# Performance work log

Hardware: AMD Instinct MI355X
Metric: run time of the kernel (lower is better)

Reference implementation:

```python
import jax, jax.numpy as jnp
import numpy as np

D_MODEL = 1024
N_HEADS = 16
MAX_SEQ_LEN = 2048

def setup_inputs() -> dict:
    key = jax.random.key(0)
    ks = jax.random.split(key, 4)
    B, L, D = 2, 2048, D_MODEL
    s = 0.02
    x = jax.random.normal(ks[0], (B, L, D), dtype=jnp.float32)
    qkv_w = jax.random.normal(ks[1], (D, 3 * D), dtype=jnp.float32) * s
    qkv_b = jnp.zeros((3 * D,), dtype=jnp.float32)
    proj_w = jax.random.normal(ks[2], (D, D), dtype=jnp.float32) * s
    proj_b = jnp.zeros((D,), dtype=jnp.float32)
    bias_table = jax.random.normal(ks[3], (2 * MAX_SEQ_LEN - 1, N_HEADS), dtype=jnp.float32) * s
    return {"x": x, "qkv_w": qkv_w, "qkv_b": qkv_b, "proj_w": proj_w, "proj_b": proj_b, "bias_table": bias_table}

def reference(x, qkv_w, qkv_b, proj_w, proj_b, bias_table):
    B, L, D = x.shape
    H = N_HEADS
    dk = D // H
    scale = dk ** -0.5
    # fused qkv projection: (B,L,3,H,dk)
    qkv = (x @ qkv_w + qkv_b).reshape(B, L, 3, H, dk)
    q = qkv[:, :, 0].transpose(0, 2, 1, 3)  # (B,H,L,dk)
    k = qkv[:, :, 1].transpose(0, 2, 1, 3)
    v = qkv[:, :, 2].transpose(0, 2, 1, 3)
    attn = jnp.einsum("bhqd,bhkd->bhqk", q, k) * scale  # (B,H,L,L)
    # relative position bias gather (Swin-style)
    coords = jnp.arange(L)
    rel_idx = coords[None, :] - coords[:, None] + (MAX_SEQ_LEN - 1)  # (L,L)
    rel_bias = bias_table[rel_idx]  # (L,L,H)
    attn = attn + rel_bias.transpose(2, 0, 1)[None]  # (B,H,L,L)
    attn = jax.nn.softmax(attn, axis=-1)
    out = jnp.einsum("bhqk,bhkd->bhqd", attn, v)  # (B,H,L,dk)
    out = out.transpose(0, 2, 1, 3).reshape(B, L, D)
    return out @ proj_w + proj_b
```

## Files before the change

### kernel.cpp

```cpp
#include <hip/hip_runtime.h>
#include <stdint.h>

typedef __attribute__((ext_vector_type(4))) float    f32x4;
typedef f32x4 __attribute__((aligned(4)))   f32x4u;
typedef __attribute__((ext_vector_type(8))) short    bf16x8;
typedef __attribute__((ext_vector_type(2))) uint32_t u32x2;
typedef __attribute__((ext_vector_type(4))) uint32_t u32x4;

#define MFMA16(a,b,c) __builtin_amdgcn_mfma_f32_16x16x32_bf16((a),(b),(c),0,0,0)

__device__ __forceinline__ uint16_t f2bf(float f){
  uint32_t u = __float_as_uint(f);
  return (uint16_t)((u + 0x7FFFu + ((u >> 16) & 1u)) >> 16);
}

__device__ __forceinline__ uint32_t pk_bf16(float lo, float hi){
  uint32_t r; asm("v_cvt_pk_bf16_f32 %0, %1, %2" : "=v"(r) : "v"(lo), "v"(hi)); return r;
}

__device__ __forceinline__ float fast_exp2(float x){
  float r; asm("v_exp_f32 %0, %1" : "=v"(r) : "v"(x)); return r;
}
__device__ __forceinline__ float fast_log2(float x){
  float r; asm("v_log_f32 %0, %1" : "=v"(r) : "v"(x)); return r;
}

__device__ __forceinline__ float bfl(uint32_t u){ return __uint_as_float(u << 16); }
__device__ __forceinline__ float bfh(uint32_t u){ return __uint_as_float(u & 0xffff0000u); }

__device__ __forceinline__ void gload16(const uint16_t* g, uint16_t* l){
  __builtin_amdgcn_global_load_lds((const __attribute__((address_space(1))) uint32_t*)g,
                                   (__attribute__((address_space(3))) uint32_t*)l, 16, 0, 0);
}

__global__ void k_cvtb(const float* __restrict__ in, uint16_t* __restrict__ out,
                       const float* __restrict__ btab, float* __restrict__ bias_t){
  const int bx = blockIdx.x;
  if (bx < 4096){
    const size_t i = (size_t)(bx*256 + threadIdx.x) * 4;
    const f32x4 v = *(const f32x4*)(in + i);
    u32x2 pk = {pk_bf16(v[0], v[1]), pk_bf16(v[2], v[3])};
    *(u32x2*)(out + i) = pk;
  } else {
    const int i = (bx - 4096)*256 + threadIdx.x;
    if (i < 4095*16) bias_t[(i & 15)*4096 + (i >> 4)] = btab[i] * 1.4426950408889634f;
  }
}

__global__ void k_tcvt(const float* __restrict__ in, uint16_t* __restrict__ out, int K, int N){
  __shared__ float tile[64][65];
  const int k0 = blockIdx.y*64, n0 = blockIdx.x*64;
  const int tc = threadIdx.x & 63, tr = threadIdx.x >> 6;
  #pragma unroll
  for (int p=0;p<16;p++){ int r = p*4 + tr; tile[r][tc] = in[(size_t)(k0+r)*N + n0 + tc]; }
  __syncthreads();
  #pragma unroll
  for (int p=0;p<16;p++){ int r = p*4 + tr; out[(size_t)(n0+r)*K + k0 + tc] = f2bf(tile[tc][r]); }
}

__global__ __launch_bounds__(256, 2) void k_gemm(
    const uint16_t* __restrict__ A, const uint16_t* __restrict__ Bt,
    const float* __restrict__ bias,
    uint16_t* __restrict__ qo, uint16_t* __restrict__ ko, uint16_t* __restrict__ vto)
{
  __shared__ __align__(16) uint16_t at[128*64];
  __shared__ __align__(16) uint16_t bt[128*64];
  const int tid = threadIdx.x;
  const int lane = tid & 63, w = tid >> 6;
  const int g = lane >> 4, li = lane & 15;
  const int wr = w >> 1, wc = w & 1;
  const int m0 = blockIdx.y * 128, n0 = blockIdx.x * 128;

  f32x4 acc[4][4] = {};

  const int srow = tid >> 3;
  const int scg  = (tid & 7) ^ (srow & 7);

  for (int kt_ = 0; kt_ < 16; kt_++){
    const int kk = kt_*64;
    __syncthreads();
    #pragma unroll
    for (int j = 0; j < 4; j++){
      gload16(A  + (size_t)(m0 + j*32 + srow)*1024 + kk + scg*8, at + (j*256+tid)*8);
      gload16(Bt + (size_t)(n0 + j*32 + srow)*1024 + kk + scg*8, bt + (j*256+tid)*8);
    }
    asm volatile("s_waitcnt vmcnt(0)" ::: "memory");
    __syncthreads();

    bf16x8 af[2][4], bfr[2][4];
    #pragma unroll
    for (int mi=0; mi<4; mi++){
      int row = wr*64 + mi*16 + li, sw = row & 7;
      af[0][mi] = *(const bf16x8*)(at + row*64 + ((g     ^ sw)*8));
      af[1][mi] = *(const bf16x8*)(at + row*64 + (((4+g) ^ sw)*8));
    }
    #pragma unroll
    for (int ni=0; ni<4; ni++){
      int row = wc*64 + ni*16 + li, sw = row & 7;
      bfr[0][ni] = *(const bf16x8*)(bt + row*64 + ((g     ^ sw)*8));
      bfr[1][ni] = *(const bf16x8*)(bt + row*64 + (((4+g) ^ sw)*8));
    }
    #pragma unroll
    for (int s=0; s<2; s++)
      #pragma unroll
      for (int mi=0; mi<4; mi++)
        #pragma unroll
        for (int ni=0; ni<4; ni++)
          acc[mi][ni] = MFMA16(af[s][mi], bfr[s][ni], acc[mi][ni]);
  }

  #pragma unroll
  for (int ni=0; ni<4; ni++){
    const int c = n0 + wc*64 + ni*16 + li;
    const float bv = bias[c];
    const int which = c >> 10, cc = c & 1023;
    const int h = cc >> 6, d = cc & 63;
    #pragma unroll
    for (int mi=0; mi<4; mi++){
      const int trow = m0 + wr*64 + mi*16 + g*4;
      const int b_ = trow >> 11, lcl = trow & 2047;
      const f32x4 v4 = acc[mi][ni];
      if (which == 0){
        uint16_t* dst = qo + (((size_t)(b_*16 + h)*2048 + lcl)*64 + d);
        #pragma unroll
        for (int r=0;r<4;r++) dst[(size_t)r*64] = f2bf((v4[r] + bv) * 0.18033688011112042f);
      } else if (which == 1){
        uint16_t* dst = ko + (((size_t)(b_*16 + h)*2048 + lcl)*64 + d);
        #pragma unroll
        for (int r=0;r<4;r++) dst[(size_t)r*64] = f2bf(v4[r] + bv);
      } else {
        u32x2 pk = {pk_bf16(v4[0]+bv, v4[1]+bv), pk_bf16(v4[2]+bv, v4[3]+bv)};
        *(u32x2*)(vto + (((size_t)(b_*16 + h)*64 + d)*2048 + lcl)) = pk;
      }
    }
  }
}

__global__ __launch_bounds__(256, 2) void k_gemm2(
    const uint16_t* __restrict__ A, const uint16_t* __restrict__ Bt,
    const float* __restrict__ bias, float* __restrict__ outf)
{
  __shared__ __align__(16) uint16_t at[128*64];
  __shared__ __align__(16) uint16_t bt[64*64];
  const int tid = threadIdx.x;
  const int lane = tid & 63, w = tid >> 6;
  const int g = lane >> 4, li = lane & 15;
  const int wr = w >> 1, wc = w & 1;
  const int m0 = blockIdx.y * 128, n0 = blockIdx.x * 64;

  f32x4 acc[4][2] = {};
  const int srow = tid >> 3;
  const int scg  = (tid & 7) ^ (srow & 7);

  for (int kt_ = 0; kt_ < 16; kt_++){
    const int kk = kt_*64;
    __syncthreads();
    #pragma unroll
    for (int j = 0; j < 4; j++)
      gload16(A  + (size_t)(m0 + j*32 + srow)*1024 + kk + scg*8, at + (j*256+tid)*8);
    #pragma unroll
    for (int j = 0; j < 2; j++)
      gload16(Bt + (size_t)(n0 + j*32 + srow)*1024 + kk + scg*8, bt + (j*256+tid)*8);
    asm volatile("s_waitcnt vmcnt(0)" ::: "memory");
    __syncthreads();

    bf16x8 af[2][4], bfr[2][2];
    #pragma unroll
    for (int mi=0; mi<4; mi++){
      int row = wr*64 + mi*16 + li, sw = row & 7;
      af[0][mi] = *(const bf16x8*)(at + row*64 + ((g     ^ sw)*8));
      af[1][mi] = *(const bf16x8*)(at + row*64 + (((4+g) ^ sw)*8));
    }
    #pragma unroll
    for (int ni=0; ni<2; ni++){
      int row = wc*32 + ni*16 + li, sw = row & 7;
      bfr[0][ni] = *(const bf16x8*)(bt + row*64 + ((g     ^ sw)*8));
      bfr[1][ni] = *(const bf16x8*)(bt + row*64 + (((4+g) ^ sw)*8));
    }
    #pragma unroll
    for (int s=0; s<2; s++)
      #pragma unroll
      for (int mi=0; mi<4; mi++)
        #pragma unroll
        for (int ni=0; ni<2; ni++)
          acc[mi][ni] = MFMA16(af[s][mi], bfr[s][ni], acc[mi][ni]);
  }

  #pragma unroll
  for (int ni=0; ni<2; ni++){
    const int c = n0 + wc*32 + ni*16 + li;
    const float bv = bias[c];
    #pragma unroll
    for (int mi=0; mi<4; mi++){
      const int trow = m0 + wr*64 + mi*16 + g*4;
      float* dst = outf + (size_t)trow*1024 + c;
      const f32x4 v4 = acc[mi][ni];
      #pragma unroll
      for (int r=0;r<4;r++) dst[(size_t)r*1024] = v4[r] + bv;
    }
  }
}

__device__ __forceinline__ void attn_tile(
    int t, bool last, int tid, int g, int li, int srow, int scg,
    const uint16_t* kbase, const uint16_t* vbase, const float* bb,
    const uint16_t* ktc, uint16_t* ktn, const uint16_t* vtc, uint16_t* vtn, uint16_t* pl,
    const bf16x8 (&qf)[2][2], bf16x8 ones,
    f32x4 (&o)[4][2], f32x4 (&o4)[2], float& mrun0, float& mrun1)
{
  const int kv0 = t*64;

  f32x4 bv5[5];
  #pragma unroll
  for (int j=0;j<5;j++)
    bv5[j] = *(const f32x4u*)(bb + kv0 + (j-1)*16 + g*4 - li);
  asm volatile("" ::: "memory");

  if (!last){
    const int kv1 = kv0 + 64;
    gload16(kbase + (size_t)(kv1+srow)*64 + scg*8,         ktn + tid*8);
    gload16(kbase + (size_t)(kv1+srow+32)*64 + scg*8,      ktn + 2048 + tid*8);
    gload16(vbase + (size_t)srow*2048 + kv1 + scg*8,       vtn + tid*8);
    gload16(vbase + (size_t)(srow+32)*2048 + kv1 + scg*8,  vtn + 2048 + tid*8);
    asm volatile("s_waitcnt vmcnt(9)" ::: "memory");
  } else {
    asm volatile("s_waitcnt vmcnt(5)" ::: "memory");
  }
  __builtin_amdgcn_s_barrier();

  f32x4 sa[4][2];
  __builtin_amdgcn_s_setprio(1);
  #pragma unroll
  for (int mf=0; mf<4; mf++){
    const int row = mf*16 + li, sw = row & 7;
    bf16x8 a0 = *(const bf16x8*)(ktc + row*64 + ((g     ^ sw)*8));
    bf16x8 a1 = *(const bf16x8*)(ktc + row*64 + (((4+g) ^ sw)*8));
    #pragma unroll
    for (int c=0;c<2;c++){
      f32x4 cfr = {};
      cfr = MFMA16(a0, qf[c][0], cfr);
      cfr = MFMA16(a1, qf[c][1], cfr);
      sa[mf][c] = cfr;
    }
  }
  __builtin_amdgcn_s_setprio(0);

  float t0 = -__builtin_inff(), t1 = -__builtin_inff();
  #pragma unroll
  for (int mf=0; mf<4; mf++){
    sa[mf][0] += bv5[mf+1];
    sa[mf][1] += bv5[mf];
    #pragma unroll
    for (int r=0; r<4; r++){
      t0 = fmaxf(t0, sa[mf][0][r]);
      t1 = fmaxf(t1, sa[mf][1][r]);
    }
  }

  const int ok = (t0 <= mrun0 + 8.f) && (t1 <= mrun1 + 8.f);
  if (!__all(ok)){
    float r0 = t0, r1 = t1;
    r0 = fmaxf(r0, __shfl_xor(r0, 16)); r0 = fmaxf(r0, __shfl_xor(r0, 32));
    r1 = fmaxf(r1, __shfl_xor(r1, 16)); r1 = fmaxf(r1, __shfl_xor(r1, 32));
    const float mn0 = fmaxf(mrun0, r0), mn1 = fmaxf(mrun1, r1);
    const float a0 = fast_exp2(mrun0 - mn0), a1 = fast_exp2(mrun1 - mn1);
    #pragma unroll
    for (int mf=0; mf<4; mf++){ o[mf][0] *= a0; o[mf][1] *= a1; }
    o4[0] *= a0; o4[1] *= a1;
    mrun0 = mn0; mrun1 = mn1;
  }

  bf16x8 av[2][4];
  #pragma unroll
  for (int s=0; s<2; s++)
    #pragma unroll
    for (int mf=0; mf<4; mf++){
      const int row = mf*16 + li, sw = row & 7;
      av[s][mf] = *(const bf16x8*)(vtc + row*64 + (((4*s+g) ^ sw)*8));
    }

  const int swp2 = 2*(li & 7);
  #pragma unroll
  for (int c=0;c<2;c++){
    const float mr = c ? mrun1 : mrun0;
    #pragma unroll
    for (int mf=0; mf<4; mf++){
      float p0 = fast_exp2(sa[mf][c][0] - mr);
      float p1 = fast_exp2(sa[mf][c][1] - mr);
      float p2 = fast_exp2(sa[mf][c][2] - mr);
      float p3 = fast_exp2(sa[mf][c][3] - mr);
      u32x2 pk = {pk_bf16(p0,p1), pk_bf16(p2,p3)};
      *(u32x2*)(pl + li*64 + (((4*mf+g) ^ swp2)*4)) = pk;
    }
    __builtin_amdgcn_s_setprio(1);
    #pragma unroll
    for (int s=0; s<2; s++){
      bf16x8 pb = *(const bf16x8*)(pl + li*64 + (((8*s+2*g) ^ swp2)*4));
      o4[c] = MFMA16(ones, pb, o4[c]);
      #pragma unroll
      for (int mf=0; mf<4; mf++)
        o[mf][c] = MFMA16(av[s][mf], pb, o[mf][c]);
    }
    __builtin_amdgcn_s_setprio(0);
  }
  __builtin_amdgcn_s_barrier();
}

__global__ __launch_bounds__(256, 2) void k_attn(
    const uint16_t* __restrict__ qg, const uint16_t* __restrict__ kg,
    const uint16_t* __restrict__ vg, const float* __restrict__ biast,
    uint16_t* __restrict__ opart, float* __restrict__ spart)
{
  __shared__ __align__(16) uint16_t kt[2][64*64];
  __shared__ __align__(16) uint16_t vt[2][64*64];
  __shared__ __align__(16) uint16_t pt[4][16*64];
  const int tid = threadIdx.x;
  const int lane = tid & 63, w = tid >> 6;
  const int g = lane >> 4, li = lane & 15;
  const int bh = blockIdx.y, h = bh & 15, b_ = bh >> 4;
  const int id = blockIdx.x;
  const int split = id & 1, qxi = id >> 1;
  const int qw = qxi*128 + w*32;
  const int tg0 = split*16;

  bf16x8 qf[2][2];
  #pragma unroll
  for (int c=0;c<2;c++){
    const uint16_t* qp = qg + ((size_t)bh*2048 + qw + c*16 + li)*64 + g*8;
    qf[c][0] = *(const bf16x8*)(qp);
    qf[c][1] = *(const bf16x8*)(qp + 32);
  }
  bf16x8 ones = (bf16x8)(short)0;
  if (li == 0){ const short v = (short)0x3F80; ones = (bf16x8){v,v,v,v,v,v,v,v}; }

  f32x4 o[4][2] = {};
  f32x4 o4[2] = {};
  float mrun0 = -__builtin_inff(), mrun1 = -__builtin_inff();

  const uint16_t* kbase = kg + (size_t)bh*(2048*64);
  const uint16_t* vbase = vg + (size_t)bh*(64*2048);
  const int srow = tid >> 3;
  const int scg  = (tid & 7) ^ (srow & 7);
  const float* bb = biast + h*4096 + 2047 - qw;
  uint16_t* pl = &pt[w][0];

  const int kvp = tg0*64;
  gload16(kbase + (size_t)(kvp+srow)*64 + scg*8,        &kt[0][tid*8]);
  gload16(kbase + (size_t)(kvp+srow+32)*64 + scg*8,     &kt[0][2048 + tid*8]);
  gload16(vbase + (size_t)srow*2048 + kvp + scg*8,      &vt[0][tid*8]);
  gload16(vbase + (size_t)(srow+32)*2048 + kvp + scg*8, &vt[0][2048 + tid*8]);

  for (int tt = 0; tt < 16; tt += 2){
    attn_tile(tg0+tt,   false,      tid, g, li, srow, scg, kbase, vbase, bb,
              &kt[0][0], &kt[1][0], &vt[0][0], &vt[1][0], pl,
              qf, ones, o, o4, mrun0, mrun1);
    attn_tile(tg0+tt+1, tt == 14,   tid, g, li, srow, scg, kbase, vbase, bb,
              &kt[1][0], &kt[0][0], &vt[1][0], &vt[0][0], pl,
              qf, ones, o, o4, mrun0, mrun1);
  }

  const float ls0 = __shfl(o4[0][0], li);
  const float ls1 = __shfl(o4[1][0], li);
  const float inv0 = 1.0f / ls0, inv1 = 1.0f / ls1;
  const float sv0 = mrun0 + fast_log2(ls0);
  const float sv1 = mrun1 + fast_log2(ls1);
  #pragma unroll
  for (int c=0;c<2;c++){
    const float inv = c ? inv1 : inv0;
    const int token = b_*2048 + qw + c*16 + li;
    if (g == 0) spart[split*65536 + token*16 + h] = c ? sv1 : sv0;
    uint16_t* dst = opart + ((size_t)(split*4096 + token))*1024 + h*64;
    #pragma unroll
    for (int mf=0; mf<4; mf++){
      u32x2 pk = {pk_bf16(o[mf][c][0]*inv, o[mf][c][1]*inv),
                  pk_bf16(o[mf][c][2]*inv, o[mf][c][3]*inv)};
      *(u32x2*)(dst + mf*16 + g*4) = pk;
    }
  }
}

__global__ void k_merge(const uint16_t* __restrict__ op, const float* __restrict__ sp,
                        uint16_t* __restrict__ ao){
  const int gid = blockIdx.x*256 + threadIdx.x;
  const int token = gid >> 7, col0 = (gid & 127) * 8, h = col0 >> 6;
  const float s0 = sp[token*16 + h], s1 = sp[65536 + token*16 + h];
  const float sm = fmaxf(s0, s1);
  float w0 = fast_exp2(s0 - sm), w1 = fast_exp2(s1 - sm);
  const float inv = 1.0f / (w0 + w1);
  w0 *= inv; w1 *= inv;
  const size_t i0 = (size_t)token*1024 + col0;
  const u32x4 a = *(const u32x4*)(op + i0);
  const u32x4 b = *(const u32x4*)(op + (size_t)4096*1024 + i0);
  u32x4 r;
  #pragma unroll
  for (int j=0;j<4;j++){
    const float e0 = w0*bfl(a[j]) + w1*bfl(b[j]);
    const float e1 = w0*bfh(a[j]) + w1*bfh(b[j]);
    r[j] = pk_bf16(e0, e1);
  }
  *(u32x4*)(ao + i0) = r;
}

extern "C" void kernel_launch(void* const* d_in, const int* in_sizes, int n_in,
                              void* d_out, int out_size, void* d_ws, size_t ws_size,
                              hipStream_t stream)
{
  const float* x      = (const float*)d_in[0];
  const float* qkv_w  = (const float*)d_in[1];
  const float* qkv_b  = (const float*)d_in[2];
  const float* proj_w = (const float*)d_in[3];
  const float* proj_b = (const float*)d_in[4];
  const float* btab   = (const float*)d_in[5];
  float* out = (float*)d_out;

  char* p = (char*)d_ws;
  uint16_t* x_bf    = (uint16_t*)(p);
  uint16_t* qkv_wt  = (uint16_t*)(p + 8388608);
  uint16_t* proj_wt = (uint16_t*)(p + 14680064);
  uint16_t* q_buf   = (uint16_t*)(p + 16777216);
  uint16_t* k_buf   = (uint16_t*)(p + 25165824);
  uint16_t* vt_buf  = (uint16_t*)(p + 33554432);
  uint16_t* ao_buf  = (uint16_t*)(p + 41943040);
  float*    bias_t  = (float*)   (p + 50331648);

  uint16_t* o_part = (uint16_t*)d_out;
  float*    s_part = (float*)p;

  k_cvtb <<<dim3(4352),  dim3(256), 0, stream>>>(x, x_bf, btab, bias_t);
  k_tcvt <<<dim3(48,16), dim3(256), 0, stream>>>(qkv_w,  qkv_wt,  1024, 3072);
  k_tcvt <<<dim3(16,16), dim3(256), 0, stream>>>(proj_w, proj_wt, 1024, 1024);

  k_gemm   <<<dim3(24,32), dim3(256), 0, stream>>>(x_bf, qkv_wt, qkv_b, q_buf, k_buf, vt_buf);
  k_attn   <<<dim3(32,32), dim3(256), 0, stream>>>(q_buf, k_buf, vt_buf, bias_t, o_part, s_part);
  k_merge  <<<dim3(2048),  dim3(256), 0, stream>>>(o_part, s_part, ao_buf);
  k_gemm2  <<<dim3(16,32), dim3(256), 0, stream>>>(ao_buf, proj_wt, proj_b, out);
}
```

Measured before the change: 124.4 us.

## Fuse split-KV merge into output projection GEMM A-tile load

Removes the separate merge kernel. The projection GEMM now reads both partial attention outputs and their log-sum-exp values directly, combines them in registers and writes the merged bf16 tile into shared memory. This drops one launch and the write and re-read of the merged activation buffer. In exchange, each of the 16 column blocks recomputes the merge for its rows, and the A-tile load becomes a synchronous register path instead of an async global-to-LDS load. Workspace buffers are also relocated so the partials no longer live in the output buffer.

```diff
diff --git a/kernel.cpp b/kernel.cpp
--- a/kernel.cpp
+++ b/kernel.cpp
@@ -137,7 +137,8 @@
 }
 
 __global__ __launch_bounds__(256, 2) void k_gemm2(
-    const uint16_t* __restrict__ A, const uint16_t* __restrict__ Bt,
+    const uint16_t* __restrict__ op, const float* __restrict__ sp,
+    const uint16_t* __restrict__ Bt,
     const float* __restrict__ bias, float* __restrict__ outf)
 {
   __shared__ __align__(16) uint16_t at[128*64];
@@ -156,11 +157,29 @@
     const int kk = kt_*64;
     __syncthreads();
     #pragma unroll
-    for (int j = 0; j < 4; j++)
-      gload16(A  + (size_t)(m0 + j*32 + srow)*1024 + kk + scg*8, at + (j*256+tid)*8);
-    #pragma unroll
     for (int j = 0; j < 2; j++)
       gload16(Bt + (size_t)(n0 + j*32 + srow)*1024 + kk + scg*8, bt + (j*256+tid)*8);
+    #pragma unroll
+    for (int j = 0; j < 4; j++){
+      const int token = m0 + j*32 + srow;
+      const float s0 = sp[token*16 + kt_];
+      const float s1 = sp[65536 + token*16 + kt_];
+      const float sm = fmaxf(s0, s1);
+      float w0 = fast_exp2(s0 - sm), w1 = fast_exp2(s1 - sm);
+      const float winv = 1.0f / (w0 + w1);
+      w0 *= winv; w1 *= winv;
+      const uint16_t* ap = op + (size_t)token*1024 + kk + scg*8;
+      const u32x4 a = *(const u32x4*)(ap);
+      const u32x4 b = *(const u32x4*)(ap + 4194304);
+      u32x4 r;
+      #pragma unroll
+      for (int e=0;e<4;e++){
+        const float e0 = w0*bfl(a[e]) + w1*bfl(b[e]);
+        const float e1 = w0*bfh(a[e]) + w1*bfh(b[e]);
+        r[e] = pk_bf16(e0, e1);
+      }
+      *(u32x4*)(at + (j*256+tid)*8) = r;
+    }
     asm volatile("s_waitcnt vmcnt(0)" ::: "memory");
     __syncthreads();
 
@@ -379,28 +398,6 @@
   }
 }
 
-__global__ void k_merge(const uint16_t* __restrict__ op, const float* __restrict__ sp,
-                        uint16_t* __restrict__ ao){
-  const int gid = blockIdx.x*256 + threadIdx.x;
-  const int token = gid >> 7, col0 = (gid & 127) * 8, h = col0 >> 6;
-  const float s0 = sp[token*16 + h], s1 = sp[65536 + token*16 + h];
-  const float sm = fmaxf(s0, s1);
-  float w0 = fast_exp2(s0 - sm), w1 = fast_exp2(s1 - sm);
-  const float inv = 1.0f / (w0 + w1);
-  w0 *= inv; w1 *= inv;
-  const size_t i0 = (size_t)token*1024 + col0;
-  const u32x4 a = *(const u32x4*)(op + i0);
-  const u32x4 b = *(const u32x4*)(op + (size_t)4096*1024 + i0);
-  u32x4 r;
-  #pragma unroll
-  for (int j=0;j<4;j++){
-    const float e0 = w0*bfl(a[j]) + w1*bfl(b[j]);
-    const float e1 = w0*bfh(a[j]) + w1*bfh(b[j]);
-    r[j] = pk_bf16(e0, e1);
-  }
-  *(u32x4*)(ao + i0) = r;
-}
-
 extern "C" void kernel_launch(void* const* d_in, const int* in_sizes, int n_in,
                               void* d_out, int out_size, void* d_ws, size_t ws_size,
                               hipStream_t stream)
@@ -416,15 +413,13 @@
   char* p = (char*)d_ws;
   uint16_t* x_bf    = (uint16_t*)(p);
   uint16_t* qkv_wt  = (uint16_t*)(p + 8388608);
-  uint16_t* proj_wt = (uint16_t*)(p + 14680064);
   uint16_t* q_buf   = (uint16_t*)(p + 16777216);
   uint16_t* k_buf   = (uint16_t*)(p + 25165824);
   uint16_t* vt_buf  = (uint16_t*)(p + 33554432);
-  uint16_t* ao_buf  = (uint16_t*)(p + 41943040);
+  uint16_t* proj_wt = (uint16_t*)(p + 41943040);
+  float*    s_part  = (float*)   (p + 44040192);
   float*    bias_t  = (float*)   (p + 50331648);
-
-  uint16_t* o_part = (uint16_t*)d_out;
-  float*    s_part = (float*)p;
+  uint16_t* o_part  = (uint16_t*)(p);
 
   k_cvtb <<<dim3(4352),  dim3(256), 0, stream>>>(x, x_bf, btab, bias_t);
   k_tcvt <<<dim3(48,16), dim3(256), 0, stream>>>(qkv_w,  qkv_wt,  1024, 3072);
@@ -432,6 +427,5 @@
 
   k_gemm   <<<dim3(24,32), dim3(256), 0, stream>>>(x_bf, qkv_wt, qkv_b, q_buf, k_buf, vt_buf);
   k_attn   <<<dim3(32,32), dim3(256), 0, stream>>>(q_buf, k_buf, vt_buf, bias_t, o_part, s_part);
-  k_merge  <<<dim3(2048),  dim3(256), 0, stream>>>(o_part, s_part, ao_buf);
-  k_gemm2  <<<dim3(16,32), dim3(256), 0, stream>>>(ao_buf, proj_wt, proj_b, out);
-}
+  k_gemm2  <<<dim3(16,32), dim3(256), 0, stream>>>(o_part, s_part, proj_wt, proj_b, out);
+}
```

Result: slower. 157.0 us (+26.2%).

## Double-buffer LDS tiles in QKV GEMM to overlap global loads with MFMA

Applied to the files above, without the earlier changes.

Splits the A and B shared-memory tiles into two buffers and issues the global-to-LDS loads for the next K tile before computing on the current one. It waits only for the older loads with a partial vmcnt wait, and uses raw s_barrier calls in place of __syncthreads. This hides global load latency behind the MFMA work. In exchange LDS use doubles to 64KB per block, which may limit the 2-blocks-per-CU target, and the barrier and waitcnt ordering has to be right for correctness.

```diff
diff --git a/kernel.cpp b/kernel.cpp
--- a/kernel.cpp
+++ b/kernel.cpp
@@ -63,8 +63,8 @@
     const float* __restrict__ bias,
     uint16_t* __restrict__ qo, uint16_t* __restrict__ ko, uint16_t* __restrict__ vto)
 {
-  __shared__ __align__(16) uint16_t at[128*64];
-  __shared__ __align__(16) uint16_t bt[128*64];
+  __shared__ __align__(16) uint16_t at[2][128*64];
+  __shared__ __align__(16) uint16_t bt[2][128*64];
   const int tid = threadIdx.x;
   const int lane = tid & 63, w = tid >> 6;
   const int g = lane >> 4, li = lane & 15;
@@ -76,29 +76,41 @@
   const int srow = tid >> 3;
   const int scg  = (tid & 7) ^ (srow & 7);
 
+  #pragma unroll
+  for (int j = 0; j < 4; j++){
+    gload16(A  + (size_t)(m0 + j*32 + srow)*1024 + scg*8, &at[0][(j*256+tid)*8]);
+    gload16(Bt + (size_t)(n0 + j*32 + srow)*1024 + scg*8, &bt[0][(j*256+tid)*8]);
+  }
+
   for (int kt_ = 0; kt_ < 16; kt_++){
-    const int kk = kt_*64;
-    __syncthreads();
-    #pragma unroll
-    for (int j = 0; j < 4; j++){
-      gload16(A  + (size_t)(m0 + j*32 + srow)*1024 + kk + scg*8, at + (j*256+tid)*8);
-      gload16(Bt + (size_t)(n0 + j*32 + srow)*1024 + kk + scg*8, bt + (j*256+tid)*8);
-    }
-    asm volatile("s_waitcnt vmcnt(0)" ::: "memory");
-    __syncthreads();
+    const int cur = kt_ & 1;
+    if (kt_ < 15){
+      const int kk1 = (kt_+1)*64;
+      #pragma unroll
+      for (int j = 0; j < 4; j++){
+        gload16(A  + (size_t)(m0 + j*32 + srow)*1024 + kk1 + scg*8, &at[cur^1][(j*256+tid)*8]);
+        gload16(Bt + (size_t)(n0 + j*32 + srow)*1024 + kk1 + scg*8, &bt[cur^1][(j*256+tid)*8]);
+      }
+      asm volatile("s_waitcnt vmcnt(8)" ::: "memory");
+    } else {
+      asm volatile("s_waitcnt vmcnt(0)" ::: "memory");
+    }
+    __builtin_amdgcn_s_barrier();
+    const uint16_t* atc = &at[cur][0];
+    const uint16_t* btc = &bt[cur][0];
 
     bf16x8 af[2][4], bfr[2][4];
     #pragma unroll
     for (int mi=0; mi<4; mi++){
       int row = wr*64 + mi*16 + li, sw = row & 7;
-      af[0][mi] = *(const bf16x8*)(at + row*64 + ((g     ^ sw)*8));
-      af[1][mi] = *(const bf16x8*)(at + row*64 + (((4+g) ^ sw)*8));
+      af[0][mi] = *(const bf16x8*)(atc + row*64 + ((g     ^ sw)*8));
+      af[1][mi] = *(const bf16x8*)(atc + row*64 + (((4+g) ^ sw)*8));
     }
     #pragma unroll
     for (int ni=0; ni<4; ni++){
       int row = wc*64 + ni*16 + li, sw = row & 7;
-      bfr[0][ni] = *(const bf16x8*)(bt + row*64 + ((g     ^ sw)*8));
-      bfr[1][ni] = *(const bf16x8*)(bt + row*64 + (((4+g) ^ sw)*8));
+      bfr[0][ni] = *(const bf16x8*)(btc + row*64 + ((g     ^ sw)*8));
+      bfr[1][ni] = *(const bf16x8*)(btc + row*64 + (((4+g) ^ sw)*8));
     }
     #pragma unroll
     for (int s=0; s<2; s++)
@@ -107,6 +119,7 @@
         #pragma unroll
         for (int ni=0; ni<4; ni++)
           acc[mi][ni] = MFMA16(af[s][mi], bfr[s][ni], acc[mi][ni]);
+    __builtin_amdgcn_s_barrier();
   }
 
   #pragma unroll
```

After: 132.8 us. 1.07x slower.

## Remove split-KV attention and merge kernel, process full key range per block

Applied to the files above, without the earlier changes.

The attention kernel no longer splits the key dimension into two halves with partial outputs and log-sum-exp values. Each block now loops over all 32 key tiles and writes the normalized bf16 output directly, so the separate merge kernel and its partial-buffer traffic go away. The cost is half as many attention blocks (512 instead of 1024 on 256 CUs at 2 blocks per CU), which lowers occupancy and parallelism, and each block runs a longer serial loop.

```diff
diff --git a/kernel.cpp b/kernel.cpp
--- a/kernel.cpp
+++ b/kernel.cpp
@@ -5,7 +5,6 @@
 typedef f32x4 __attribute__((aligned(4)))   f32x4u;
 typedef __attribute__((ext_vector_type(8))) short    bf16x8;
 typedef __attribute__((ext_vector_type(2))) uint32_t u32x2;
-typedef __attribute__((ext_vector_type(4))) uint32_t u32x4;
 
 #define MFMA16(a,b,c) __builtin_amdgcn_mfma_f32_16x16x32_bf16((a),(b),(c),0,0,0)
 
@@ -21,12 +20,6 @@
 __device__ __forceinline__ float fast_exp2(float x){
   float r; asm("v_exp_f32 %0, %1" : "=v"(r) : "v"(x)); return r;
 }
-__device__ __forceinline__ float fast_log2(float x){
-  float r; asm("v_log_f32 %0, %1" : "=v"(r) : "v"(x)); return r;
-}
-
-__device__ __forceinline__ float bfl(uint32_t u){ return __uint_as_float(u << 16); }
-__device__ __forceinline__ float bfh(uint32_t u){ return __uint_as_float(u & 0xffff0000u); }
 
 __device__ __forceinline__ void gload16(const uint16_t* g, uint16_t* l){
   __builtin_amdgcn_global_load_lds((const __attribute__((address_space(1))) uint32_t*)g,
@@ -309,7 +302,7 @@
 __global__ __launch_bounds__(256, 2) void k_attn(
     const uint16_t* __restrict__ qg, const uint16_t* __restrict__ kg,
     const uint16_t* __restrict__ vg, const float* __restrict__ biast,
-    uint16_t* __restrict__ opart, float* __restrict__ spart)
+    uint16_t* __restrict__ outp)
 {
   __shared__ __align__(16) uint16_t kt[2][64*64];
   __shared__ __align__(16) uint16_t vt[2][64*64];
@@ -318,10 +311,7 @@
   const int lane = tid & 63, w = tid >> 6;
   const int g = lane >> 4, li = lane & 15;
   const int bh = blockIdx.y, h = bh & 15, b_ = bh >> 4;
-  const int id = blockIdx.x;
-  const int split = id & 1, qxi = id >> 1;
-  const int qw = qxi*128 + w*32;
-  const int tg0 = split*16;
+  const int qw = blockIdx.x*128 + w*32;
 
   bf16x8 qf[2][2];
   #pragma unroll
@@ -344,17 +334,16 @@
   const float* bb = biast + h*4096 + 2047 - qw;
   uint16_t* pl = &pt[w][0];
 
-  const int kvp = tg0*64;
-  gload16(kbase + (size_t)(kvp+srow)*64 + scg*8,        &kt[0][tid*8]);
-  gload16(kbase + (size_t)(kvp+srow+32)*64 + scg*8,     &kt[0][2048 + tid*8]);
-  gload16(vbase + (size_t)srow*2048 + kvp + scg*8,      &vt[0][tid*8]);
-  gload16(vbase + (size_t)(srow+32)*2048 + kvp + scg*8, &vt[0][2048 + tid*8]);
-
-  for (int tt = 0; tt < 16; tt += 2){
-    attn_tile(tg0+tt,   false,      tid, g, li, srow, scg, kbase, vbase, bb,
+  gload16(kbase + (size_t)srow*64 + scg*8,         &kt[0][tid*8]);
+  gload16(kbase + (size_t)(srow+32)*64 + scg*8,    &kt[0][2048 + tid*8]);
+  gload16(vbase + (size_t)srow*2048 + scg*8,       &vt[0][tid*8]);
+  gload16(vbase + (size_t)(srow+32)*2048 + scg*8,  &vt[0][2048 + tid*8]);
+
+  for (int tt = 0; tt < 32; tt += 2){
+    attn_tile(tt,   false,    tid, g, li, srow, scg, kbase, vbase, bb,
               &kt[0][0], &kt[1][0], &vt[0][0], &vt[1][0], pl,
               qf, ones, o, o4, mrun0, mrun1);
-    attn_tile(tg0+tt+1, tt == 14,   tid, g, li, srow, scg, kbase, vbase, bb,
+    attn_tile(tt+1, tt == 30, tid, g, li, srow, scg, kbase, vbase, bb,
               &kt[1][0], &kt[0][0], &vt[1][0], &vt[0][0], pl,
               qf, ones, o, o4, mrun0, mrun1);
   }
@@ -362,43 +351,17 @@
   const float ls0 = __shfl(o4[0][0], li);
   const float ls1 = __shfl(o4[1][0], li);
   const float inv0 = 1.0f / ls0, inv1 = 1.0f / ls1;
-  const float sv0 = mrun0 + fast_log2(ls0);
-  const float sv1 = mrun1 + fast_log2(ls1);
   #pragma unroll
   for (int c=0;c<2;c++){
     const float inv = c ? inv1 : inv0;
-    const int token = b_*2048 + qw + c*16 + li;
-    if (g == 0) spart[split*65536 + token*16 + h] = c ? sv1 : sv0;
-    uint16_t* dst = opart + ((size_t)(split*4096 + token))*1024 + h*64;
+    const size_t token = (size_t)b_*2048 + qw + c*16 + li;
     #pragma unroll
     for (int mf=0; mf<4; mf++){
       u32x2 pk = {pk_bf16(o[mf][c][0]*inv, o[mf][c][1]*inv),
                   pk_bf16(o[mf][c][2]*inv, o[mf][c][3]*inv)};
-      *(u32x2*)(dst + mf*16 + g*4) = pk;
-    }
-  }
-}
-
-__global__ void k_merge(const uint16_t* __restrict__ op, const float* __restrict__ sp,
-                        uint16_t* __restrict__ ao){
-  const int gid = blockIdx.x*256 + threadIdx.x;
-  const int token = gid >> 7, col0 = (gid & 127) * 8, h = col0 >> 6;
-  const float s0 = sp[token*16 + h], s1 = sp[65536 + token*16 + h];
-  const float sm = fmaxf(s0, s1);
-  float w0 = fast_exp2(s0 - sm), w1 = fast_exp2(s1 - sm);
-  const float inv = 1.0f / (w0 + w1);
-  w0 *= inv; w1 *= inv;
-  const size_t i0 = (size_t)token*1024 + col0;
-  const u32x4 a = *(const u32x4*)(op + i0);
-  const u32x4 b = *(const u32x4*)(op + (size_t)4096*1024 + i0);
-  u32x4 r;
-  #pragma unroll
-  for (int j=0;j<4;j++){
-    const float e0 = w0*bfl(a[j]) + w1*bfl(b[j]);
-    const float e1 = w0*bfh(a[j]) + w1*bfh(b[j]);
-    r[j] = pk_bf16(e0, e1);
-  }
-  *(u32x4*)(ao + i0) = r;
+      *(u32x2*)(outp + token*1024 + h*64 + mf*16 + g*4) = pk;
+    }
+  }
 }
 
 extern "C" void kernel_launch(void* const* d_in, const int* in_sizes, int n_in,
@@ -423,15 +386,11 @@
   uint16_t* ao_buf  = (uint16_t*)(p + 41943040);
   float*    bias_t  = (float*)   (p + 50331648);
 
-  uint16_t* o_part = (uint16_t*)d_out;
-  float*    s_part = (float*)p;
-
   k_cvtb <<<dim3(4352),  dim3(256), 0, stream>>>(x, x_bf, btab, bias_t);
   k_tcvt <<<dim3(48,16), dim3(256), 0, stream>>>(qkv_w,  qkv_wt,  1024, 3072);
   k_tcvt <<<dim3(16,16), dim3(256), 0, stream>>>(proj_w, proj_wt, 1024, 1024);
 
   k_gemm   <<<dim3(24,32), dim3(256), 0, stream>>>(x_bf, qkv_wt, qkv_b, q_buf, k_buf, vt_buf);
-  k_attn   <<<dim3(32,32), dim3(256), 0, stream>>>(q_buf, k_buf, vt_buf, bias_t, o_part, s_part);
-  k_merge  <<<dim3(2048),  dim3(256), 0, stream>>>(o_part, s_part, ao_buf);
+  k_attn   <<<dim3(16,32), dim3(256), 0, stream>>>(q_buf, k_buf, vt_buf, bias_t, ao_buf);
   k_gemm2  <<<dim3(16,32), dim3(256), 0, stream>>>(ao_buf, proj_wt, proj_b, out);
 }
```

New measurement: 119.5 us. -3.9%, faster.
